# Performance work log

Measured on AMD Instinct MI355X. Metric: run time of the kernel, lower is better.

The kernel has to match this reference:

```python
import jax, jax.numpy as jnp
import numpy as np

B, S, D = 2, 1024, 768
H, DH = 12, 64
M = 64            # performer random features
DFF = 4 * D
EPS_LN = 1e-5
EPS_PHI = 1e-6


def setup_inputs() -> dict:
    key = jax.random.key(0)
    ks = jax.random.split(key, 12)
    std = 0.02
    return {
        "x": jax.random.normal(ks[0], (B, S, D), jnp.float32),
        "ln1_g": jnp.ones((D,), jnp.float32),
        "ln1_b": jnp.zeros((D,), jnp.float32),
        "w_attn": jax.random.normal(ks[1], (D, 3 * D), jnp.float32) * std,
        "b_attn": jnp.zeros((3 * D,), jnp.float32),
        "w_feat": jax.random.normal(ks[2], (M, DH), jnp.float32),  # FAVOR+ projection
        "w_proj": jax.random.normal(ks[3], (D, D), jnp.float32) * std,
        "b_proj": jnp.zeros((D,), jnp.float32),
        "ln2_g": jnp.ones((D,), jnp.float32),
        "ln2_b": jnp.zeros((D,), jnp.float32),
        "w_fc": jax.random.normal(ks[4], (D, DFF), jnp.float32) * std,
        "b_fc": jnp.zeros((DFF,), jnp.float32),
        "w_out": jax.random.normal(ks[5], (DFF, D), jnp.float32) * std,
        "b_out": jnp.zeros((D,), jnp.float32),
    }


def _layernorm(x, g, b):
    mu = jnp.mean(x, axis=-1, keepdims=True)
    var = jnp.mean(jnp.square(x - mu), axis=-1, keepdims=True)
    return (x - mu) * jax.lax.rsqrt(var + EPS_LN) * g + b


def _phi(x, w_feat):
    # FAVOR+ positive softmax-kernel features. x: [B,H,S,DH] (already scaled by dh^-1/4)
    proj = jnp.einsum('bhsd,md->bhsm', x, w_feat)
    sq = 0.5 * jnp.sum(jnp.square(x), axis=-1, keepdims=True)
    return jnp.exp(proj - sq) / np.sqrt(M) + EPS_PHI


def _performer_attn(q, k, v, w_feat, w_proj, b_proj):
    # split heads: [B,S,D] -> [B,H,S,DH]
    def heads(t):
        return t.reshape(B, S, H, DH).transpose(0, 2, 1, 3)
    q, k, v = heads(q), heads(k), heads(v)
    scale = DH ** -0.25
    phi_q = _phi(q * scale, w_feat)  # [B,H,S,M]
    phi_k = _phi(k * scale, w_feat)
    # causal linear attention via prefix sums
    kv = jnp.cumsum(phi_k[..., :, None] * v[..., None, :], axis=2)  # [B,H,S,M,DH]
    num = jnp.einsum('bhsm,bhsmd->bhsd', phi_q, kv)
    den = jnp.einsum('bhsm,bhsm->bhs', phi_q, jnp.cumsum(phi_k, axis=2))
    out = num / den[..., None]
    out = out.transpose(0, 2, 1, 3).reshape(B, S, D)
    return out @ w_proj + b_proj


def reference(x, ln1_g, ln1_b, w_attn, b_attn, w_feat, w_proj, b_proj,
              ln2_g, ln2_b, w_fc, b_fc, w_out, b_out):
    a = _layernorm(x, ln1_g, ln1_b)
    qkv = a @ w_attn + b_attn                      # TFConv1D
    q, k, v = jnp.split(qkv, 3, axis=2)
    x = x + _performer_attn(q, k, v, w_feat, w_proj, b_proj)
    m = _layernorm(x, ln2_g, ln2_b)
    m = jax.nn.gelu(m @ w_fc + b_fc, approximate=True) @ w_out + b_out
    return x + m
```

## Files before the change

kernel.cpp:

```cpp
#include <hip/hip_runtime.h>
#include <hip/hip_bf16.h>
#include <math.h>

#define BB 2
#define SS 1024
#define DD 768
#define HH 12
#define DHH 64
#define MM 64
#define DFF 3072
#define BS (BB*SS)
#define EPS_LN 1e-5f
#define EPS_PHI 1e-6f
#define CC 64
#define NC (SS/CC)
#define NQ 3840
#define PQOFF 2304
#define PKOFF 3072
#define VOFF  1536

typedef __hip_bfloat16 bf16;
using v8s = __attribute__((ext_vector_type(8))) short;
using v4f = __attribute__((ext_vector_type(4))) float;
struct b4 { bf16 v[4]; };

typedef const __attribute__((address_space(1))) void ga_void;
typedef __attribute__((address_space(3))) void ls_void;
__device__ __forceinline__ void gload16(const void* g, void* l) {
    __builtin_amdgcn_global_load_lds((ga_void*)g, (ls_void*)l, 16, 0, 0);
}

__global__ __launch_bounds__(256) void transpose_all_kernel(const float* __restrict__ w_attn,
                                                            const float* __restrict__ w_proj,
                                                            const float* __restrict__ w_fc,
                                                            const float* __restrict__ w_out,
                                                            bf16* __restrict__ wext_t,
                                                            bf16* __restrict__ wproj_t,
                                                            bf16* __restrict__ wfc_t,
                                                            bf16* __restrict__ wout_t) {
    int bid = blockIdx.x;
    const float* in; bf16* outp; int K, N, xt, yt;
    if (bid < 1728)      { in = w_attn; outp = wext_t;  K = 768;  N = 2304; xt = bid % 72;          yt = bid / 72; }
    else if (bid < 2304) { int b = bid - 1728; in = w_proj; outp = wproj_t; K = 768;  N = 768;  xt = b % 24; yt = b / 24; }
    else if (bid < 4608) { int b = bid - 2304; in = w_fc;   outp = wfc_t;   K = 768;  N = 3072; xt = b % 96; yt = b / 96; }
    else                 { int b = bid - 4608; in = w_out;  outp = wout_t;  K = 3072; N = 768;  xt = b % 24; yt = b / 24; }
    __shared__ float t[32][33];
    int tx = threadIdx.x & 31, ty = threadIdx.x >> 5;
    int n0 = xt * 32, k0 = yt * 32;
    #pragma unroll
    for (int i = ty; i < 32; i += 8)
        t[i][tx] = in[(size_t)(k0 + i) * N + n0 + tx];
    __syncthreads();
    #pragma unroll
    for (int i = ty; i < 32; i += 8)
        outp[(size_t)(n0 + i) * K + k0 + tx] = __float2bfloat16(t[tx][i]);
}

__global__ __launch_bounds__(256) void fuse_feat_kernel(const float* __restrict__ w_attn,
                                                        const float* __restrict__ b_attn,
                                                        const float* __restrict__ wfeat,
                                                        bf16* __restrict__ bt_ext,
                                                        float* __restrict__ bias_ext) {
    __shared__ float wfT[64][65];
    __shared__ float Wt[64][65];
    int t = threadIdx.x;
    int j0 = blockIdx.x * 64, h = blockIdx.y, isK = blockIdx.z;
    int base = isK * DD + h * DHH;
    const float scale = 0.35355339059327373f;
    #pragma unroll
    for (int it = 0; it < 16; it++) {
        int idx = it * 256 + t;
        int m = idx >> 6, d = idx & 63;
        wfT[d][m] = scale * wfeat[m * DHH + d];
        Wt[idx >> 6][idx & 63] = w_attn[(size_t)(j0 + (idx >> 6)) * (3 * DD) + base + (idx & 63)];
    }
    __syncthreads();
    int jl = t & 63, mg = (t >> 6) * 16;
    for (int m = mg; m < mg + 16; m++) {
        float acc = 0.f;
        #pragma unroll 8
        for (int d = 0; d < 64; d++) acc += wfT[d][m] * Wt[jl][d];
        bt_ext[(size_t)(PQOFF + isK * DD + h * DHH + m) * DD + j0 + jl] = __float2bfloat16(acc);
    }
    if (blockIdx.x == 0 && t < 64) {
        float accb = 0.f;
        #pragma unroll 8
        for (int d = 0; d < 64; d++) accb += wfT[d][t] * b_attn[base + d];
        bias_ext[PQOFF + isK * DD + h * DHH + t] = accb;
    }
}

__global__ __launch_bounds__(256) void ln_kernel(const float* __restrict__ x,
                                                 const float* __restrict__ g,
                                                 const float* __restrict__ bta,
                                                 bf16* __restrict__ out) {
    int row = blockIdx.x;
    int t = threadIdx.x;
    const float* xr = x + (size_t)row * DD;
    float v0 = xr[t], v1 = xr[t + 256], v2 = xr[t + 512];
    float s = v0 + v1 + v2;
    float s2 = v0 * v0 + v1 * v1 + v2 * v2;
    #pragma unroll
    for (int off = 32; off > 0; off >>= 1) {
        s  += __shfl_xor(s,  off, 64);
        s2 += __shfl_xor(s2, off, 64);
    }
    __shared__ float ls[4], ls2[4];
    if ((t & 63) == 0) { ls[t >> 6] = s; ls2[t >> 6] = s2; }
    __syncthreads();
    s  = ls[0] + ls[1] + ls[2] + ls[3];
    s2 = ls2[0] + ls2[1] + ls2[2] + ls2[3];
    float mu  = s * (1.0f / DD);
    float var = s2 * (1.0f / DD) - mu * mu;
    float r = rsqrtf(var + EPS_LN);
    bf16* orow = out + (size_t)row * DD;
    orow[t]       = __float2bfloat16((v0 - mu) * r * g[t]       + bta[t]);
    orow[t + 256] = __float2bfloat16((v1 - mu) * r * g[t + 256] + bta[t + 256]);
    orow[t + 512] = __float2bfloat16((v2 - mu) * r * g[t + 512] + bta[t + 512]);
}

__device__ inline void swizzle44(int bid, int nx4, int& bx, int& by) {
    int g = bid >> 4, r = bid & 15;
    bx = (g % nx4) * 4 + (r & 3);
    by = (g / nx4) * 4 + (r >> 2);
}

__device__ inline float gelu_tanh(float x) {
    float x3 = x * x * x;
    float u = 0.7978845608028654f * (x + 0.044715f * x3);
    return 0.5f * x * (1.0f + tanhf(u));
}

template <int ACT, int HAS_RES, int OUT_BF16>
__global__ __launch_bounds__(256) void gemm_k128(const bf16* __restrict__ A,
                                                 const bf16* __restrict__ BT,
                                                 const float* __restrict__ bias,
                                                 const float* __restrict__ res,
                                                 void* __restrict__ Cout,
                                                 int N, int K, int nx4) {
    __shared__ bf16 Asl[64][128];
    __shared__ bf16 Bsl[64][128];
    int bx, by;
    swizzle44(blockIdx.x, nx4, bx, by);
    int tid = threadIdx.x;
    int m0 = by * 64, n0 = bx * 64;
    int wave = tid >> 6, lane = tid & 63;
    int qm = lane & 15, quad = lane >> 4;
    int srow = lane >> 4;
    int chnk = lane & 15;
    int sce = (chnk ^ srow) * 8;
    int sco = (chnk ^ (srow + 4)) * 8;
    const bf16* ag = A  + (size_t)(m0 + wave * 16 + srow) * K;
    const bf16* bg = BT + (size_t)(n0 + wave * 16 + srow) * K;
    int xr = (qm & 7) << 3;

    v4f acc[4] = {{0.f,0.f,0.f,0.f},{0.f,0.f,0.f,0.f},{0.f,0.f,0.f,0.f},{0.f,0.f,0.f,0.f}};

    for (int k0 = 0; k0 < K; k0 += 128) {
        __syncthreads();
        #pragma unroll
        for (int i = 0; i < 4; i++) {
            int sc = (i & 1) ? sco : sce;
            gload16(ag + (size_t)(4 * i) * K + k0 + sc, &Asl[wave * 16 + 4 * i][0]);
            gload16(bg + (size_t)(4 * i) * K + k0 + sc, &Bsl[wave * 16 + 4 * i][0]);
        }
        __syncthreads();
        #pragma unroll
        for (int kc = 0; kc < 4; kc++) {
            v8s a = *(const v8s*)&Asl[wave * 16 + qm][(kc * 32 + quad * 8) ^ xr];
            #pragma unroll
            for (int n = 0; n < 4; n++) {
                v8s b = *(const v8s*)&Bsl[n * 16 + qm][(kc * 32 + quad * 8) ^ xr];
                acc[n] = __builtin_amdgcn_mfma_f32_16x16x32_bf16(a, b, acc[n], 0, 0, 0);
            }
        }
    }

    int col_l = lane & 15;
    #pragma unroll
    for (int t = 0; t < 4; t++) {
        int col = n0 + t * 16 + col_l;
        float bcol = bias[col];
        #pragma unroll
        for (int r = 0; r < 4; r++) {
            int row = m0 + wave * 16 + quad * 4 + r;
            float v = acc[t][r] + bcol;
            if (ACT == 1) v = gelu_tanh(v);
            if (HAS_RES) v += res[(size_t)row * N + col];
            if (OUT_BF16) ((bf16*)Cout)[(size_t)row * N + col] = __float2bfloat16(v);
            else          ((float*)Cout)[(size_t)row * N + col] = v;
        }
    }
}

template <int ACT, int HAS_RES, int OUT_BF16>
__global__ __launch_bounds__(256) void gemm_m32_k128(const bf16* __restrict__ A,
                                                     const bf16* __restrict__ BT,
                                                     const float* __restrict__ bias,
                                                     const float* __restrict__ res,
                                                     void* __restrict__ Cout,
                                                     int N, int K, int nx4) {
    __shared__ bf16 Asl[32][128];
    __shared__ bf16 Bsl[64][128];
    int bx, by;
    swizzle44(blockIdx.x, nx4, bx, by);
    int tid = threadIdx.x;
    int m0 = by * 32, n0 = bx * 64;
    int wave = tid >> 6, lane = tid & 63;
    int qm = lane & 15, quad = lane >> 4;
    int rowh = (wave & 1) * 16;
    int colh = (wave >> 1) * 32;
    int srow = lane >> 4;
    int chnk = lane & 15;
    int sce = (chnk ^ srow) * 8;
    int sco = (chnk ^ (srow + 4)) * 8;
    const bf16* ag = A  + (size_t)(m0 + wave * 8  + srow) * K;
    const bf16* bg = BT + (size_t)(n0 + wave * 16 + srow) * K;
    int xr = (qm & 7) << 3;

    v4f acc[2] = {{0.f,0.f,0.f,0.f},{0.f,0.f,0.f,0.f}};

    for (int k0 = 0; k0 < K; k0 += 128) {
        __syncthreads();
        #pragma unroll
        for (int i = 0; i < 2; i++) {
            int sc = (i & 1) ? sco : sce;
            gload16(ag + (size_t)(4 * i) * K + k0 + sc, &Asl[wave * 8 + 4 * i][0]);
        }
        #pragma unroll
        for (int i = 0; i < 4; i++) {
            int sc = (i & 1) ? sco : sce;
            gload16(bg + (size_t)(4 * i) * K + k0 + sc, &Bsl[wave * 16 + 4 * i][0]);
        }
        __syncthreads();
        #pragma unroll
        for (int kc = 0; kc < 4; kc++) {
            v8s a  = *(const v8s*)&Asl[rowh + qm][(kc * 32 + quad * 8) ^ xr];
            v8s b0 = *(const v8s*)&Bsl[colh + qm][(kc * 32 + quad * 8) ^ xr];
            v8s b1 = *(const v8s*)&Bsl[colh + 16 + qm][(kc * 32 + quad * 8) ^ xr];
            acc[0] = __builtin_amdgcn_mfma_f32_16x16x32_bf16(a, b0, acc[0], 0, 0, 0);
            acc[1] = __builtin_amdgcn_mfma_f32_16x16x32_bf16(a, b1, acc[1], 0, 0, 0);
        }
    }

    #pragma unroll
    for (int ct = 0; ct < 2; ct++) {
        int col = n0 + colh + ct * 16 + qm;
        float bcol = bias[col];
        #pragma unroll
        for (int r = 0; r < 4; r++) {
            int row = m0 + rowh + quad * 4 + r;
            float v = acc[ct][r] + bcol;
            if (ACT == 1) v = gelu_tanh(v);
            if (HAS_RES) v += res[(size_t)row * N + col];
            if (OUT_BF16) ((bf16*)Cout)[(size_t)row * N + col] = __float2bfloat16(v);
            else          ((float*)Cout)[(size_t)row * N + col] = v;
        }
    }
}

__global__ __launch_bounds__(256) void phi_exp_kernel(bf16* __restrict__ qkvp) {
    int s = blockIdx.x, z = blockIdx.z;
    int b = z >> 1, isK = z & 1;
    int t = threadIdx.x;
    int h = blockIdx.y * 4 + (t >> 6);
    int m = t & 63;
    size_t row = (size_t)b * SS + s;
    float qd = __bfloat162float(qkvp[row * NQ + isK * DD + h * DHH + m]);
    float sq = qd * qd;
    #pragma unroll
    for (int off = 32; off > 0; off >>= 1) sq += __shfl_xor(sq, off, 64);
    sq *= (1.0f / 16.0f);
    size_t pidx = row * NQ + PQOFF + isK * DD + h * DHH + m;
    float proj = __bfloat162float(qkvp[pidx]);
    qkvp[pidx] = __float2bfloat16(__expf(proj - sq) * 0.125f + EPS_PHI);
}

__global__ __launch_bounds__(256) void scan_sums_mfma(const bf16* __restrict__ qkvp,
                                                      float* __restrict__ StateT,
                                                      float* __restrict__ Sk) {
    int c = blockIdx.x, h = blockIdx.y, b = blockIdx.z;
    int bh = b * HH + h;
    int t = threadIdx.x;
    __shared__ bf16 vt[64][72];
    __shared__ bf16 kt[64][72];
    int sr = t >> 4, cq = (t & 15) * 4;
    #pragma unroll
    for (int i = 0; i < 4; i++) {
        int s = sr + 16 * i;
        size_t rowg = ((size_t)b * SS + c * CC + s) * NQ + h * DHH;
        b4 vv = *(const b4*)&qkvp[rowg + VOFF  + cq];
        b4 kv = *(const b4*)&qkvp[rowg + PKOFF + cq];
        #pragma unroll
        for (int j = 0; j < 4; j++) {
            vt[cq + j][s] = vv.v[j];
            kt[cq + j][s] = kv.v[j];
        }
    }
    __syncthreads();
    int wave = t >> 6, lane = t & 63, qm = lane & 15, quad = lane >> 4;
    v4f acc[4] = {{0.f,0.f,0.f,0.f},{0.f,0.f,0.f,0.f},{0.f,0.f,0.f,0.f},{0.f,0.f,0.f,0.f}};
    #pragma unroll
    for (int k0 = 0; k0 < 64; k0 += 32) {
        v8s a = *(const v8s*)&vt[wave * 16 + qm][k0 + quad * 8];
        #pragma unroll
        for (int n = 0; n < 4; n++) {
            v8s bb = *(const v8s*)&kt[n * 16 + qm][k0 + quad * 8];
            acc[n] = __builtin_amdgcn_mfma_f32_16x16x32_bf16(a, bb, acc[n], 0, 0, 0);
        }
    }
    float* dst = StateT + ((size_t)bh * NC + c) * 4096;
    int col_l = lane & 15;
    #pragma unroll
    for (int n = 0; n < 4; n++)
        #pragma unroll
        for (int r = 0; r < 4; r++) {
            int d = wave * 16 + quad * 4 + r;
            dst[d * 64 + n * 16 + col_l] = acc[n][r];
        }
    if (t < 64) {
        float sum = 0.f;
        #pragma unroll 8
        for (int i = 0; i < 64; i++) sum += __bfloat162float(kt[t][i]);
        Sk[((size_t)bh * NC + c) * 64 + t] = sum;
    }
}

__global__ __launch_bounds__(256) void scan_prefix_kernel(float* __restrict__ Skv,
                                                          float* __restrict__ Sk) {
    int bh = blockIdx.y;
    int t = blockIdx.x * 256 + threadIdx.x;
    size_t base = (size_t)bh * NC * 4096 + t;
    float acc = 0.f;
    for (int c = 0; c < NC; c++) {
        float v = Skv[base + (size_t)c * 4096];
        Skv[base + (size_t)c * 4096] = acc;
        acc += v;
    }
    if (blockIdx.x == 0 && threadIdx.x < 64) {
        size_t b2 = (size_t)bh * NC * 64 + threadIdx.x;
        float a2 = 0.f;
        for (int c = 0; c < NC; c++) {
            float v = Sk[b2 + (size_t)c * 64];
            Sk[b2 + (size_t)c * 64] = a2;
            a2 += v;
        }
    }
}

__global__ __launch_bounds__(256) void scan_chunk_mfma(const bf16* __restrict__ qkvp,
                                                       const float* __restrict__ StateT,
                                                       const float* __restrict__ SkPre,
                                                       bf16* __restrict__ attn) {
    int c = blockIdx.x, h = blockIdx.y, b = blockIdx.z;
    int bh = b * HH + h;
    int t = threadIdx.x;
    __shared__ bf16 qs[64][72];
    __shared__ bf16 ks[64][72];
    __shared__ bf16 vt[80][72];
    __shared__ bf16 stl[80][72];
    __shared__ bf16 P[64][72];
    int sr = t >> 4, cq = (t & 15) * 4;
    const float* stg = StateT + ((size_t)bh * NC + c) * 4096;
    #pragma unroll
    for (int i = 0; i < 4; i++) {
        int s = sr + 16 * i;
        size_t rowg = ((size_t)b * SS + c * CC + s) * NQ + h * DHH;
        b4 qv = *(const b4*)&qkvp[rowg + PQOFF + cq];
        b4 kv = *(const b4*)&qkvp[rowg + PKOFF + cq];
        b4 vv = *(const b4*)&qkvp[rowg + VOFF  + cq];
        float4 sv = *(const float4*)&stg[s * 64 + cq];
        #pragma unroll
        for (int j = 0; j < 4; j++) {
            qs[s][cq + j] = qv.v[j];
            ks[s][cq + j] = kv.v[j];
            vt[cq + j][s] = vv.v[j];
        }
        stl[s][cq + 0] = __float2bfloat16(sv.x);
        stl[s][cq + 1] = __float2bfloat16(sv.y);
        stl[s][cq + 2] = __float2bfloat16(sv.z);
        stl[s][cq + 3] = __float2bfloat16(sv.w);
    }
    {
        int rr = 64 + (t >> 4);
        bf16 one = __float2bfloat16(rr == 64 ? 1.f : 0.f);
        vt[rr][cq + 0] = one; vt[rr][cq + 1] = one;
        vt[rr][cq + 2] = one; vt[rr][cq + 3] = one;
        if (rr == 64) {
            const float* skp = SkPre + ((size_t)bh * NC + c) * 64;
            float4 s4 = *(const float4*)&skp[cq];
            stl[64][cq + 0] = __float2bfloat16(s4.x);
            stl[64][cq + 1] = __float2bfloat16(s4.y);
            stl[64][cq + 2] = __float2bfloat16(s4.z);
            stl[64][cq + 3] = __float2bfloat16(s4.w);
        } else {
            bf16 z = __float2bfloat16(0.f);
            stl[rr][cq + 0] = z; stl[rr][cq + 1] = z;
            stl[rr][cq + 2] = z; stl[rr][cq + 3] = z;
        }
    }
    __syncthreads();
    int wave = t >> 6, lane = t & 63, qm = lane & 15, quad = lane >> 4;
    int col_l = lane & 15;
    int row0 = wave * 16;

    v4f a1[4] = {{0.f,0.f,0.f,0.f},{0.f,0.f,0.f,0.f},{0.f,0.f,0.f,0.f},{0.f,0.f,0.f,0.f}};
    #pragma unroll
    for (int k0 = 0; k0 < 64; k0 += 32) {
        v8s a = *(const v8s*)&qs[row0 + qm][k0 + quad * 8];
        #pragma unroll
        for (int n = 0; n < 4; n++) {
            v8s bb = *(const v8s*)&ks[n * 16 + qm][k0 + quad * 8];
            a1[n] = __builtin_amdgcn_mfma_f32_16x16x32_bf16(a, bb, a1[n], 0, 0, 0);
        }
    }
    #pragma unroll
    for (int n = 0; n < 4; n++)
        #pragma unroll
        for (int r = 0; r < 4; r++) {
            int row = row0 + quad * 4 + r;
            int col = n * 16 + col_l;
            float v = (col <= row) ? a1[n][r] : 0.f;
            P[row][col] = __float2bfloat16(v);
        }
    v4f acc[5] = {{0.f,0.f,0.f,0.f},{0.f,0.f,0.f,0.f},{0.f,0.f,0.f,0.f},
                  {0.f,0.f,0.f,0.f},{0.f,0.f,0.f,0.f}};
    #pragma unroll
    for (int k0 = 0; k0 < 64; k0 += 32) {
        v8s aq = *(const v8s*)&qs[row0 + qm][k0 + quad * 8];
        v8s ap = *(const v8s*)&P [row0 + qm][k0 + quad * 8];
        #pragma unroll
        for (int n = 0; n < 5; n++) {
            v8s b1 = *(const v8s*)&stl[n * 16 + qm][k0 + quad * 8];
            v8s b2 = *(const v8s*)&vt [n * 16 + qm][k0 + quad * 8];
            acc[n] = __builtin_amdgcn_mfma_f32_16x16x32_bf16(aq, b1, acc[n], 0, 0, 0);
            acc[n] = __builtin_amdgcn_mfma_f32_16x16x32_bf16(ap, b2, acc[n], 0, 0, 0);
        }
    }
    float den[4];
    #pragma unroll
    for (int r = 0; r < 4; r++)
        den[r] = __shfl(acc[4][r], (lane >> 4) << 4, 64);
    #pragma unroll
    for (int n = 0; n < 4; n++)
        #pragma unroll
        for (int r = 0; r < 4; r++) {
            int srow = row0 + quad * 4 + r;
            int d = n * 16 + col_l;
            attn[((size_t)b * SS + c * CC + srow) * DD + h * DHH + d] =
                __float2bfloat16(acc[n][r] / den[r]);
        }
}

extern "C" void kernel_launch(void* const* d_in, const int* in_sizes, int n_in,
                              void* d_out, int out_size, void* d_ws, size_t ws_size,
                              hipStream_t stream) {
    const float* x      = (const float*)d_in[0];
    const float* ln1_g  = (const float*)d_in[1];
    const float* ln1_b  = (const float*)d_in[2];
    const float* w_attn = (const float*)d_in[3];
    const float* b_attn = (const float*)d_in[4];
    const float* w_feat = (const float*)d_in[5];
    const float* w_proj = (const float*)d_in[6];
    const float* b_proj = (const float*)d_in[7];
    const float* ln2_g  = (const float*)d_in[8];
    const float* ln2_b  = (const float*)d_in[9];
    const float* w_fc   = (const float*)d_in[10];
    const float* b_fc   = (const float*)d_in[11];
    const float* w_out  = (const float*)d_in[12];
    const float* b_out  = (const float*)d_in[13];
    float* out = (float*)d_out;

    float* ws = (float*)d_ws;
    size_t off = 0;
    float* buf_x1   = ws + off; off += (size_t)BS * DD;
    float* buf_sk   = ws + off; off += (size_t)BB * HH * NC * MM;
    float* bias_ext = ws + off; off += NQ;
    bf16* wb = (bf16*)(ws + off);
    size_t boff = 0;
    bf16* buf_qkvp    = wb + boff; boff += (size_t)BS * NQ;
    bf16* buf_a_bf    = wb + boff; boff += (size_t)BS * DD;
    bf16* buf_attn_bf = wb + boff; boff += (size_t)BS * DD;
    bf16* wext_t      = wb + boff; boff += (size_t)NQ * DD;
    bf16* wproj_t     = wb + boff; boff += (size_t)DD * DD;
    bf16* wfc_t       = wb + boff; boff += (size_t)DFF * DD;
    bf16* wout_t      = wb + boff; boff += (size_t)DD * DFF;
    float* buf_skv   = buf_x1;
    bf16*  buf_fc_bf = buf_qkvp;

    transpose_all_kernel<<<6912, 256, 0, stream>>>(w_attn, w_proj, w_fc, w_out,
                                                   wext_t, wproj_t, wfc_t, wout_t);
    fuse_feat_kernel<<<dim3(DD / 64, HH, 2), 256, 0, stream>>>(w_attn, b_attn, w_feat, wext_t, bias_ext);
    hipMemcpyAsync(bias_ext, b_attn, 3 * DD * sizeof(float), hipMemcpyDeviceToDevice, stream);

    ln_kernel<<<BS, 256, 0, stream>>>(x, ln1_g, ln1_b, buf_a_bf);
    gemm_k128<0, 0, 1><<<1920, 256, 0, stream>>>(
        buf_a_bf, wext_t, bias_ext, nullptr, buf_qkvp, NQ, DD, 15);
    phi_exp_kernel<<<dim3(SS, 3, 2 * BB), 256, 0, stream>>>(buf_qkvp);
    scan_sums_mfma<<<dim3(NC, HH, BB), 256, 0, stream>>>(buf_qkvp, buf_skv, buf_sk);
    scan_prefix_kernel<<<dim3(4096 / 256, BB * HH), 256, 0, stream>>>(buf_skv, buf_sk);
    scan_chunk_mfma<<<dim3(NC, HH, BB), 256, 0, stream>>>(
        buf_qkvp, buf_skv, buf_sk, buf_attn_bf);
    gemm_m32_k128<0, 1, 0><<<768, 256, 0, stream>>>(
        buf_attn_bf, wproj_t, b_proj, x, buf_x1, DD, DD, 3);
    ln_kernel<<<BS, 256, 0, stream>>>(buf_x1, ln2_g, ln2_b, buf_a_bf);
    gemm_k128<1, 0, 1><<<1536, 256, 0, stream>>>(
        buf_a_bf, wfc_t, b_fc, nullptr, buf_fc_bf, DFF, DD, 12);
    gemm_m32_k128<0, 1, 0><<<768, 256, 0, stream>>>(
        buf_fc_bf, wout_t, b_out, buf_x1, out, DD, DFF, 3);
}
```

Baseline: 230.7 us.

## Fuse phi exp into scan kernels and merge weight prep launches

Removes the standalone phi_exp kernel and recomputes the FAVOR+ exp features (with the per-row squared norm reduced over 16 lanes) while loading tiles in scan_sums and scan_chunk. Merges the transpose, feature-fusion and bias-copy steps into one prep kernel launch. This removes a read-modify-write pass over the qkvp buffer and two launches. In exchange, the k features are computed twice and more raw data is loaded per tile.

```diff
diff --git a/kernel.cpp b/kernel.cpp
--- a/kernel.cpp
+++ b/kernel.cpp
@@ -30,63 +30,67 @@
     __builtin_amdgcn_global_load_lds((ga_void*)g, (ls_void*)l, 16, 0, 0);
 }
 
-__global__ __launch_bounds__(256) void transpose_all_kernel(const float* __restrict__ w_attn,
-                                                            const float* __restrict__ w_proj,
-                                                            const float* __restrict__ w_fc,
-                                                            const float* __restrict__ w_out,
-                                                            bf16* __restrict__ wext_t,
-                                                            bf16* __restrict__ wproj_t,
-                                                            bf16* __restrict__ wfc_t,
-                                                            bf16* __restrict__ wout_t) {
+__global__ __launch_bounds__(256) void prep_kernel(const float* __restrict__ w_attn,
+                                                   const float* __restrict__ w_proj,
+                                                   const float* __restrict__ w_fc,
+                                                   const float* __restrict__ w_out,
+                                                   const float* __restrict__ b_attn,
+                                                   const float* __restrict__ wfeat,
+                                                   bf16* __restrict__ wext_t,
+                                                   bf16* __restrict__ wproj_t,
+                                                   bf16* __restrict__ wfc_t,
+                                                   bf16* __restrict__ wout_t,
+                                                   float* __restrict__ bias_ext) {
+    __shared__ float smem[2 * 64 * 65];
     int bid = blockIdx.x;
-    const float* in; bf16* outp; int K, N, xt, yt;
-    if (bid < 1728)      { in = w_attn; outp = wext_t;  K = 768;  N = 2304; xt = bid % 72;          yt = bid / 72; }
-    else if (bid < 2304) { int b = bid - 1728; in = w_proj; outp = wproj_t; K = 768;  N = 768;  xt = b % 24; yt = b / 24; }
-    else if (bid < 4608) { int b = bid - 2304; in = w_fc;   outp = wfc_t;   K = 768;  N = 3072; xt = b % 96; yt = b / 96; }
-    else                 { int b = bid - 4608; in = w_out;  outp = wout_t;  K = 3072; N = 768;  xt = b % 24; yt = b / 24; }
-    __shared__ float t[32][33];
-    int tx = threadIdx.x & 31, ty = threadIdx.x >> 5;
-    int n0 = xt * 32, k0 = yt * 32;
-    #pragma unroll
-    for (int i = ty; i < 32; i += 8)
-        t[i][tx] = in[(size_t)(k0 + i) * N + n0 + tx];
-    __syncthreads();
-    #pragma unroll
-    for (int i = ty; i < 32; i += 8)
-        outp[(size_t)(n0 + i) * K + k0 + tx] = __float2bfloat16(t[tx][i]);
-}
-
-__global__ __launch_bounds__(256) void fuse_feat_kernel(const float* __restrict__ w_attn,
-                                                        const float* __restrict__ b_attn,
-                                                        const float* __restrict__ wfeat,
-                                                        bf16* __restrict__ bt_ext,
-                                                        float* __restrict__ bias_ext) {
-    __shared__ float wfT[64][65];
-    __shared__ float Wt[64][65];
     int t = threadIdx.x;
-    int j0 = blockIdx.x * 64, h = blockIdx.y, isK = blockIdx.z;
-    int base = isK * DD + h * DHH;
-    const float scale = 0.35355339059327373f;
-    #pragma unroll
-    for (int it = 0; it < 16; it++) {
-        int idx = it * 256 + t;
-        int m = idx >> 6, d = idx & 63;
-        wfT[d][m] = scale * wfeat[m * DHH + d];
-        Wt[idx >> 6][idx & 63] = w_attn[(size_t)(j0 + (idx >> 6)) * (3 * DD) + base + (idx & 63)];
-    }
-    __syncthreads();
-    int jl = t & 63, mg = (t >> 6) * 16;
-    for (int m = mg; m < mg + 16; m++) {
-        float acc = 0.f;
-        #pragma unroll 8
-        for (int d = 0; d < 64; d++) acc += wfT[d][m] * Wt[jl][d];
-        bt_ext[(size_t)(PQOFF + isK * DD + h * DHH + m) * DD + j0 + jl] = __float2bfloat16(acc);
-    }
-    if (blockIdx.x == 0 && t < 64) {
-        float accb = 0.f;
-        #pragma unroll 8
-        for (int d = 0; d < 64; d++) accb += wfT[d][t] * b_attn[base + d];
-        bias_ext[PQOFF + isK * DD + h * DHH + t] = accb;
+    if (bid < 6912) {
+        const float* in; bf16* outp; int K, N, xt, yt;
+        if (bid < 1728)      { in = w_attn; outp = wext_t;  K = 768;  N = 2304; xt = bid % 72;          yt = bid / 72; }
+        else if (bid < 2304) { int b = bid - 1728; in = w_proj; outp = wproj_t; K = 768;  N = 768;  xt = b % 24; yt = b / 24; }
+        else if (bid < 4608) { int b = bid - 2304; in = w_fc;   outp = wfc_t;   K = 768;  N = 3072; xt = b % 96; yt = b / 96; }
+        else                 { int b = bid - 4608; in = w_out;  outp = wout_t;  K = 3072; N = 768;  xt = b % 24; yt = b / 24; }
+        float (*tt)[33] = (float(*)[33])smem;
+        int tx = t & 31, ty = t >> 5;
+        int n0 = xt * 32, k0 = yt * 32;
+        #pragma unroll
+        for (int i = ty; i < 32; i += 8)
+            tt[i][tx] = in[(size_t)(k0 + i) * N + n0 + tx];
+        __syncthreads();
+        #pragma unroll
+        for (int i = ty; i < 32; i += 8)
+            outp[(size_t)(n0 + i) * K + k0 + tx] = __float2bfloat16(tt[tx][i]);
+    } else if (bid < 7200) {
+        int b2 = bid - 6912;
+        int jb = b2 % 12, h = (b2 / 12) % 12, isK = b2 / 144;
+        float (*wfT)[65] = (float(*)[65])smem;
+        float (*Wt)[65]  = (float(*)[65])(smem + 64 * 65);
+        int j0 = jb * 64;
+        int base = isK * DD + h * DHH;
+        const float scale = 0.35355339059327373f;
+        #pragma unroll
+        for (int it = 0; it < 16; it++) {
+            int idx = it * 256 + t;
+            int m = idx >> 6, d = idx & 63;
+            wfT[d][m] = scale * wfeat[m * DHH + d];
+            Wt[idx >> 6][idx & 63] = w_attn[(size_t)(j0 + (idx >> 6)) * (3 * DD) + base + (idx & 63)];
+        }
+        __syncthreads();
+        int jl = t & 63, mg = (t >> 6) * 16;
+        for (int m = mg; m < mg + 16; m++) {
+            float acc = 0.f;
+            #pragma unroll 8
+            for (int d = 0; d < 64; d++) acc += wfT[d][m] * Wt[jl][d];
+            wext_t[(size_t)(PQOFF + isK * DD + h * DHH + m) * DD + j0 + jl] = __float2bfloat16(acc);
+        }
+        if (jb == 0 && t < 64) {
+            float accb = 0.f;
+            #pragma unroll 8
+            for (int d = 0; d < 64; d++) accb += wfT[d][t] * b_attn[base + d];
+            bias_ext[PQOFF + isK * DD + h * DHH + t] = accb;
+        }
+    } else {
+        for (int i = t; i < 3 * DD; i += 256) bias_ext[i] = b_attn[i];
     }
 }
 
@@ -259,21 +263,13 @@
     }
 }
 
-__global__ __launch_bounds__(256) void phi_exp_kernel(bf16* __restrict__ qkvp) {
-    int s = blockIdx.x, z = blockIdx.z;
-    int b = z >> 1, isK = z & 1;
-    int t = threadIdx.x;
-    int h = blockIdx.y * 4 + (t >> 6);
-    int m = t & 63;
-    size_t row = (size_t)b * SS + s;
-    float qd = __bfloat162float(qkvp[row * NQ + isK * DD + h * DHH + m]);
-    float sq = qd * qd;
-    #pragma unroll
-    for (int off = 32; off > 0; off >>= 1) sq += __shfl_xor(sq, off, 64);
-    sq *= (1.0f / 16.0f);
-    size_t pidx = row * NQ + PQOFF + isK * DD + h * DHH + m;
-    float proj = __bfloat162float(qkvp[pidx]);
-    qkvp[pidx] = __float2bfloat16(__expf(proj - sq) * 0.125f + EPS_PHI);
+__device__ __forceinline__ float rowsq16(b4 raw) {
+    float sq = 0.f;
+    #pragma unroll
+    for (int j = 0; j < 4; j++) { float f = __bfloat162float(raw.v[j]); sq += f * f; }
+    sq += __shfl_xor(sq, 1, 64); sq += __shfl_xor(sq, 2, 64);
+    sq += __shfl_xor(sq, 4, 64); sq += __shfl_xor(sq, 8, 64);
+    return sq * (1.0f / 16.0f);
 }
 
 __global__ __launch_bounds__(256) void scan_sums_mfma(const bf16* __restrict__ qkvp,
@@ -290,11 +286,14 @@
         int s = sr + 16 * i;
         size_t rowg = ((size_t)b * SS + c * CC + s) * NQ + h * DHH;
         b4 vv = *(const b4*)&qkvp[rowg + VOFF  + cq];
-        b4 kv = *(const b4*)&qkvp[rowg + PKOFF + cq];
+        b4 kr = *(const b4*)&qkvp[rowg + DD    + cq];
+        b4 kp = *(const b4*)&qkvp[rowg + PKOFF + cq];
+        float sq = rowsq16(kr);
         #pragma unroll
         for (int j = 0; j < 4; j++) {
             vt[cq + j][s] = vv.v[j];
-            kt[cq + j][s] = kv.v[j];
+            kt[cq + j][s] = __float2bfloat16(
+                __expf(__bfloat162float(kp.v[j]) - sq) * 0.125f + EPS_PHI);
         }
     }
     __syncthreads();
@@ -366,14 +365,20 @@
     for (int i = 0; i < 4; i++) {
         int s = sr + 16 * i;
         size_t rowg = ((size_t)b * SS + c * CC + s) * NQ + h * DHH;
-        b4 qv = *(const b4*)&qkvp[rowg + PQOFF + cq];
-        b4 kv = *(const b4*)&qkvp[rowg + PKOFF + cq];
+        b4 qr = *(const b4*)&qkvp[rowg + 0     + cq];
+        b4 qp = *(const b4*)&qkvp[rowg + PQOFF + cq];
+        b4 kr = *(const b4*)&qkvp[rowg + DD    + cq];
+        b4 kp = *(const b4*)&qkvp[rowg + PKOFF + cq];
         b4 vv = *(const b4*)&qkvp[rowg + VOFF  + cq];
         float4 sv = *(const float4*)&stg[s * 64 + cq];
+        float sqq = rowsq16(qr);
+        float sqk = rowsq16(kr);
         #pragma unroll
         for (int j = 0; j < 4; j++) {
-            qs[s][cq + j] = qv.v[j];
-            ks[s][cq + j] = kv.v[j];
+            qs[s][cq + j] = __float2bfloat16(
+                __expf(__bfloat162float(qp.v[j]) - sqq) * 0.125f + EPS_PHI);
+            ks[s][cq + j] = __float2bfloat16(
+                __expf(__bfloat162float(kp.v[j]) - sqk) * 0.125f + EPS_PHI);
             vt[cq + j][s] = vv.v[j];
         }
         stl[s][cq + 0] = __float2bfloat16(sv.x);
@@ -488,15 +493,11 @@
     float* buf_skv   = buf_x1;
     bf16*  buf_fc_bf = buf_qkvp;
 
-    transpose_all_kernel<<<6912, 256, 0, stream>>>(w_attn, w_proj, w_fc, w_out,
-                                                   wext_t, wproj_t, wfc_t, wout_t);
-    fuse_feat_kernel<<<dim3(DD / 64, HH, 2), 256, 0, stream>>>(w_attn, b_attn, w_feat, wext_t, bias_ext);
-    hipMemcpyAsync(bias_ext, b_attn, 3 * DD * sizeof(float), hipMemcpyDeviceToDevice, stream);
-
+    prep_kernel<<<7201, 256, 0, stream>>>(w_attn, w_proj, w_fc, w_out, b_attn, w_feat,
+                                          wext_t, wproj_t, wfc_t, wout_t, bias_ext);
     ln_kernel<<<BS, 256, 0, stream>>>(x, ln1_g, ln1_b, buf_a_bf);
     gemm_k128<0, 0, 1><<<1920, 256, 0, stream>>>(
         buf_a_bf, wext_t, bias_ext, nullptr, buf_qkvp, NQ, DD, 15);
-    phi_exp_kernel<<<dim3(SS, 3, 2 * BB), 256, 0, stream>>>(buf_qkvp);
     scan_sums_mfma<<<dim3(NC, HH, BB), 256, 0, stream>>>(buf_qkvp, buf_skv, buf_sk);
     scan_prefix_kernel<<<dim3(4096 / 256, BB * HH), 256, 0, stream>>>(buf_skv, buf_sk);
     scan_chunk_mfma<<<dim3(NC, HH, BB), 256, 0, stream>>>(
```

Measured after the change: 235.8 us. 1.02x slower.
